# Kernel tuning notes

Measured on AMD Instinct MI355X. Metric: run time of the kernel, lower is better.

The kernel has to match this reference:

```python
import jax, jax.numpy as jnp
import numpy as np

SPATIAL_SCALE = 0.125  # stride-8 FPN level
POINTS = 5


def _sample_points(bb):
    # bb: [N,H,W,5] = (cx, cy, w, h, theta) in image coords
    cx, cy, w, h, t = [bb[..., i] for i in range(5)]
    if POINTS == 1:
        px = cx[..., None]
        py = cy[..., None]
    else:
        vx = w * jnp.cos(t) * 0.5
        vy = w * jnp.sin(t) * 0.5
        wx = -h * jnp.sin(t) * 0.5
        wy = h * jnp.cos(t) * 0.5
        px = jnp.stack([cx, cx + vx + wx, cx - vx + wx, cx - vx - wx, cx + vx - wx], axis=-1)
        py = jnp.stack([cy, cy + vy + wy, cy - vy + wy, cy - vy - wy, cy + vy - wy], axis=-1)
    return px * SPATIAL_SCALE, py * SPATIAL_SCALE  # [N,H,W,P] feature-map coords


def _bilinear_gather(feat, y, x):
    # feat: [N,C,H,W]; y,x: [N,H,W,P] -> [N,H,W,P,C], mmcv-style bilinear w/ border rules
    N, C, H, W = feat.shape
    valid = (y >= -1.0) & (y <= H) & (x >= -1.0) & (x <= W)
    y = jnp.maximum(y, 0.0)
    x = jnp.maximum(x, 0.0)
    y_low = jnp.minimum(jnp.floor(y).astype(jnp.int32), H - 1)
    x_low = jnp.minimum(jnp.floor(x).astype(jnp.int32), W - 1)
    # if low index hits last row/col, snap coordinate onto it (ly/lx = 0)
    y = jnp.where(y_low >= H - 1, y_low.astype(feat.dtype), y)
    x = jnp.where(x_low >= W - 1, x_low.astype(feat.dtype), x)
    y_high = jnp.minimum(y_low + 1, H - 1)
    x_high = jnp.minimum(x_low + 1, W - 1)
    ly = y - y_low.astype(feat.dtype)
    lx = x - x_low.astype(feat.dtype)
    hy = 1.0 - ly
    hx = 1.0 - lx
    nn = jnp.arange(N)[:, None, None, None]  # broadcasts against [N,H,W,P]

    def g(yy, xx):
        return feat[nn, :, yy, xx]  # [N,H,W,P,C]

    val = ((hy * hx)[..., None] * g(y_low, x_low)
           + (hy * lx)[..., None] * g(y_low, x_high)
           + (ly * hx)[..., None] * g(y_high, x_low)
           + (ly * lx)[..., None] * g(y_high, x_high))
    return jnp.where(valid[..., None], val, 0.0)


def feature_refine(features, best_rbboxes):
    px, py = _sample_points(best_rbboxes)
    sampled = _bilinear_gather(features, py, px)       # [N,H,W,P,C]
    acc = sampled.sum(axis=3)                           # [N,H,W,C]
    return features + jnp.transpose(acc, (0, 3, 1, 2))  # [N,C,H,W]


def setup_inputs() -> dict:
    key = jax.random.key(0)
    k1, k2, k3, k4, k5, k6 = jax.random.split(key, 6)
    N, C, H, W = 4, 256, 128, 128
    IMG = 1024.0
    features = jax.random.normal(k1, (N, C, H, W), dtype=jnp.float32)
    cx = jax.random.uniform(k2, (N, H, W), minval=0.0, maxval=IMG)
    cy = jax.random.uniform(k3, (N, H, W), minval=0.0, maxval=IMG)
    bw = jax.random.uniform(k4, (N, H, W), minval=8.0, maxval=128.0)
    bh = jax.random.uniform(k5, (N, H, W), minval=8.0, maxval=128.0)
    th = jax.random.uniform(k6, (N, H, W), minval=-np.pi / 2, maxval=np.pi / 2)
    best_rbboxes = jnp.stack([cx, cy, bw, bh, th], axis=-1)  # [N,H,W,5]
    return {"features": features, "best_rbboxes": best_rbboxes}


def reference(features, best_rbboxes):
    return feature_refine(features, best_rbboxes)
```

## Files before the change

### kernel.cpp

```cpp
#include <hip/hip_runtime.h>


#define N_ 4
#define C_ 256
#define H_ 128
#define W_ 128
#define HW_ (H_ * W_)
#define SCALE 0.125f

typedef unsigned int uint32;
typedef float f32x2 __attribute__((ext_vector_type(2)));

__device__ __forceinline__ uint32 f2bf(float f) {
    uint32 u = __float_as_uint(f);
    u = (u + 0x7FFF + ((u >> 16) & 1)) >> 16;
    return u;
}
__device__ __forceinline__ float blo(uint32 u) { return __uint_as_float(u << 16); }
__device__ __forceinline__ float bhi(uint32 u) { return __uint_as_float(u & 0xFFFF0000u); }

__global__ __launch_bounds__(1024, 8) void nchw2nhwc_geo(const float* __restrict__ in,
                                                         const float* __restrict__ bb,
                                                         uint32* __restrict__ outU,
                                                         uint32* __restrict__ geoG)
{
    __shared__ uint32 tile[64 * 260];
    const int t   = threadIdx.x;
    const int l   = t & 63;
    const int g   = t >> 6;
    const int hw0 = blockIdx.x * 256;
    const int ch  = blockIdx.y;
    const int n   = blockIdx.z;

    if (ch == 0 && t < 256) {
        const int px = n * HW_ + hw0 + t;
        const float* b = bb + (size_t)px * 5;
        const float cx = b[0], cy = b[1], bw = b[2], bh = b[3], th = b[4];
        const float st = sinf(th), ct = cosf(th);
        const float vx = bw * ct * 0.5f, vy = bw * st * 0.5f;
        const float wx = -bh * st * 0.5f, wy = bh * ct * 0.5f;
        const float pxs[5] = {cx, cx + vx + wx, cx - vx + wx, cx - vx - wx, cx + vx - wx};
        const float pys[5] = {cy, cy + vy + wy, cy - vy + wy, cy - vy - wy, cy + vy - wy};
        uint32* gw = geoG + (size_t)px * 40;
#pragma unroll
        for (int p = 0; p < 5; ++p) {
            float x = pxs[p] * SCALE;
            float y = pys[p] * SCALE;
            const bool valid = (y >= -1.0f) && (y <= (float)H_) &&
                               (x >= -1.0f) && (x <= (float)W_);
            y = fmaxf(y, 0.0f);
            x = fmaxf(x, 0.0f);
            int yl = min((int)y, H_ - 1);
            int xl = min((int)x, W_ - 1);
            if (yl >= H_ - 1) y = (float)yl;
            if (xl >= W_ - 1) x = (float)xl;
            const int yh = min(yl + 1, H_ - 1);
            const float ly = y - (float)yl, lx = x - (float)xl;
            const float hy = 1.0f - ly,     hx = 1.0f - lx;
            const int xa = min(xl, W_ - 2);
            float wA, wB;
            if (xl < W_ - 1) { wA = hx; wB = lx; }
            else             { wA = 0.0f; wB = 1.0f; }
            const float v = valid ? 1.0f : 0.0f;
            const int pix0 = yl * W_ + xa;
            const int pix1 = yh * W_ + xa;
            *(uint4*)&gw[p * 8]     = make_uint4((uint32)(pix0 * 512),
                                                 __float_as_uint(v * hy * wA),
                                                 (uint32)((pix0 + 1) * 512),
                                                 __float_as_uint(v * hy * wB));
            *(uint4*)&gw[p * 8 + 4] = make_uint4((uint32)(pix1 * 512),
                                                 __float_as_uint(v * ly * wA),
                                                 (uint32)((pix1 + 1) * 512),
                                                 __float_as_uint(v * ly * wB));
        }
    }

    const float* base = in + (size_t)n * C_ * HW_ + (size_t)(ch * 128) * HW_ + hw0 + 4 * l;
    float4 v0[4], v1[4];
#pragma unroll
    for (int r = 0; r < 4; ++r) {
        const int cp = g * 4 + r;
        v0[r] = *(const float4*)(base + (size_t)(2 * cp) * HW_);
        v1[r] = *(const float4*)(base + (size_t)(2 * cp + 1) * HW_);
    }
#pragma unroll
    for (int r = 0; r < 4; ++r) {
        const int cp = g * 4 + r;
        uint4 u;
        u.x = f2bf(v0[r].x) | (f2bf(v1[r].x) << 16);
        u.y = f2bf(v0[r].y) | (f2bf(v1[r].y) << 16);
        u.z = f2bf(v0[r].z) | (f2bf(v1[r].z) << 16);
        u.w = f2bf(v0[r].w) | (f2bf(v1[r].w) << 16);
        *(uint4*)&tile[cp * 260 + 4 * l] = u;
    }
    __syncthreads();
    uint32* dst = outU + ((size_t)n * HW_ + hw0) * 128 + ch * 64;
#pragma unroll
    for (int it = 0; it < 16; ++it) {
        const int f   = it * 1024 + t;
        const int row = f >> 6;
        const int q   = f & 63;
        dst[(size_t)row * 128 + q] = tile[q * 260 + row];
    }
}

__global__ __launch_bounds__(256, 8) void fr_refine(const uint32* __restrict__ nhwcU,
                                                    const uint32* __restrict__ geoG,
                                                    float* __restrict__ out)
{
    __shared__ float tile[32 * 128];
    const int t  = threadIdx.x;
    const int l  = t & 63;
    const int wv = __builtin_amdgcn_readfirstlane(t >> 6);
    const int bx = blockIdx.x;
    const int xcd = bx & 7;
    const int n   = xcd >> 1;
    const int ch  = xcd & 1;
    const int s   = bx >> 3;
    const int h   = s >> 2;
    const int w0  = (s & 3) * 32;

    const int k8   = (l >> 4) << 3;
    const int slot = (l & 15) << 4;
    const int hwb  = h * W_ + w0 + wv * 8;
    const char* gbase = (const char*)geoG + (size_t)(n * HW_ + hwb) * 160;
    const char* plane = (const char*)(nhwcU + (size_t)n * HW_ * 128) + (ch << 8);

#pragma unroll 1
    for (int p = 0; p < 8; ++p) {
        const char* gq = gbase + p * 160;

        uint2 ow[5];
#pragma unroll
        for (int q = 0; q < 5; ++q)
            ow[q] = *(const uint2*)(gq + q * 32 + k8);

        uint4 rid = make_uint4(0u, 0u, 0u, 0u);
        if (l < 16)
            rid = *(const uint4*)(plane + (size_t)(hwb + p) * 512 + slot);
        uint4 r[5];
#pragma unroll
        for (int q = 0; q < 5; ++q)
            r[q] = *(const uint4*)(plane + ow[q].x + slot);
        __builtin_amdgcn_sched_barrier(0);

        f32x2 acc0, acc1, acc2, acc3;
        acc0.x = blo(rid.x); acc0.y = bhi(rid.x);
        acc1.x = blo(rid.y); acc1.y = bhi(rid.y);
        acc2.x = blo(rid.z); acc2.y = bhi(rid.z);
        acc3.x = blo(rid.w); acc3.y = bhi(rid.w);
#pragma unroll
        for (int q = 0; q < 5; ++q) {
            const float w = __uint_as_float(ow[q].y);
            f32x2 w2; w2.x = w; w2.y = w;
            f32x2 u;
            u.x = blo(r[q].x); u.y = bhi(r[q].x); acc0 += u * w2;
            u.x = blo(r[q].y); u.y = bhi(r[q].y); acc1 += u * w2;
            u.x = blo(r[q].z); u.y = bhi(r[q].z); acc2 += u * w2;
            u.x = blo(r[q].w); u.y = bhi(r[q].w); acc3 += u * w2;
        }
        float a[8] = {acc0.x, acc0.y, acc1.x, acc1.y,
                      acc2.x, acc2.y, acc3.x, acc3.y};
#pragma unroll
        for (int k = 0; k < 8; ++k) {
            a[k] += __shfl_xor(a[k], 16, 64);
            a[k] += __shfl_xor(a[k], 32, 64);
        }
        if (l < 16) {
            const int px  = wv * 8 + p;
            const int swz = (px & 7) << 2;
            float* base = &tile[px * 128];
            *(float4*)&base[(l * 8) ^ swz]     = make_float4(a[0], a[1], a[2], a[3]);
            *(float4*)&base[(l * 8 + 4) ^ swz] = make_float4(a[4], a[5], a[6], a[7]);
        }
    }
    __syncthreads();
    const size_t obase = (size_t)n * C_ * HW_ + (size_t)(ch * 128) * HW_ + h * W_ + w0;
#pragma unroll
    for (int it = 0; it < 16; ++it) {
        const int flat = it * 256 + t;
        const int px = flat & 31;
        const int c  = flat >> 5;
        out[obase + (size_t)c * HW_ + px] = tile[px * 128 + (c ^ ((px & 7) << 2))];
    }
}

__global__ __launch_bounds__(256) void fr_kernel(
    const float* __restrict__ feat,
    const float* __restrict__ bb,
    float* __restrict__ out)
{
    const int lane = threadIdx.x & 63;
    const int wave = threadIdx.x >> 6;
    const int tile = blockIdx.x;
    const int wt   = tile & 1;
    const int h    = (tile >> 1) & (H_ - 1);
    const int n    = tile >> 8;
    const int w    = wt * 64 + lane;
    const int cb   = blockIdx.y;

    const float* b = bb + (size_t)((n * H_ + h) * W_ + w) * 5;
    const float cx = b[0], cy = b[1], bw = b[2], bh = b[3], th = b[4];
    const float st = sinf(th), ct = cosf(th);
    const float vx = bw * ct * 0.5f, vy = bw * st * 0.5f;
    const float wx = -bh * st * 0.5f, wy = bh * ct * 0.5f;
    const float pxs[5] = {cx, cx + vx + wx, cx - vx + wx, cx - vx - wx, cx + vx - wx};
    const float pys[5] = {cy, cy + vy + wy, cy - vy + wy, cy - vy - wy, cy + vy - wy};

    int   off0[5], off1[5];
    float wgt[20];
#pragma unroll
    for (int p = 0; p < 5; ++p) {
        float x = pxs[p] * SCALE;
        float y = pys[p] * SCALE;
        const bool valid = (y >= -1.0f) && (y <= (float)H_) &&
                           (x >= -1.0f) && (x <= (float)W_);
        y = fmaxf(y, 0.0f);
        x = fmaxf(x, 0.0f);
        int yl = min((int)y, H_ - 1);
        int xl = min((int)x, W_ - 1);
        if (yl >= H_ - 1) y = (float)yl;
        if (xl >= W_ - 1) x = (float)xl;
        const int yh = min(yl + 1, H_ - 1);
        const float ly = y - (float)yl, lx = x - (float)xl;
        const float hy = 1.0f - ly,     hx = 1.0f - lx;
        const int xa = min(xl, W_ - 2);
        float wA, wB;
        if (xl < W_ - 1) { wA = hx; wB = lx; }
        else             { wA = 0.0f; wB = 1.0f; }
        const float v = valid ? 1.0f : 0.0f;
        off0[p] = yl * W_ + xa;
        off1[p] = yh * W_ + xa;
        wgt[p * 4 + 0] = v * hy * wA;
        wgt[p * 4 + 1] = v * hy * wB;
        wgt[p * 4 + 2] = v * ly * wA;
        wgt[p * 4 + 3] = v * ly * wB;
    }

    const int hw = h * W_ + w;
    const size_t planeBase = ((size_t)n * C_ + cb * 64 + wave * 16) * HW_;
    const float* fp = feat + planeBase;
    float*       op = out  + planeBase;
    for (int it = 0; it < 16; ++it) {
        float acc = fp[hw];
#pragma unroll
        for (int p = 0; p < 5; ++p) {
            acc += wgt[p * 4 + 0] * fp[off0[p]]
                 + wgt[p * 4 + 1] * fp[off0[p] + 1]
                 + wgt[p * 4 + 2] * fp[off1[p]]
                 + wgt[p * 4 + 3] * fp[off1[p] + 1];
        }
        op[hw] = acc;
        fp += HW_;
        op += HW_;
    }
}

extern "C" void kernel_launch(void* const* d_in, const int* in_sizes, int n_in,
                              void* d_out, int out_size, void* d_ws, size_t ws_size,
                              hipStream_t stream) {
    const float* feat = (const float*)d_in[0];
    const float* bbox = (const float*)d_in[1];
    float* out = (float*)d_out;

    const size_t nhwcBytes = (size_t)N_ * HW_ * C_ * 2;
    const size_t geoBytes  = (size_t)N_ * HW_ * 160;
    if (ws_size >= nhwcBytes + geoBytes) {
        uint32* nhwcU = (uint32*)d_ws;
        uint32* geoG  = (uint32*)((char*)d_ws + nhwcBytes);
        nchw2nhwc_geo<<<dim3(HW_ / 256, 2, N_), dim3(1024), 0, stream>>>(feat, bbox, nhwcU, geoG);
        fr_refine<<<dim3(N_ * H_ * (W_ / 32) * 2), dim3(256), 0, stream>>>(nhwcU, geoG, out);
    } else {
        dim3 grid(N_ * H_ * (W_ / 64), C_ / 64, 1);
        fr_kernel<<<grid, dim3(256), 0, stream>>>(feat, bbox, out);
    }
}
```

Before: 167.4 us.

## Software-pipeline gather loads in refine kernel and vectorize NHWC transpose stores

The refine kernel's pixel loop is fully unrolled and software-pipelined. Geometry offsets are prefetched two iterations ahead and feature gathers one iteration ahead, so global-load latency overlaps the FMA and shuffle reduction of the current pixel. This raises register use, so launch bounds drop from 8 to 4 blocks per SM, trading occupancy for instruction-level overlap. Separately, the NCHW-to-NHWC transpose kernel now writes 16-byte uint4 stores in place of scalar stores, reducing store instruction count.

Result: no change. 166.5 us (-0.5%).

```diff
diff --git a/kernel.cpp b/kernel.cpp
--- a/kernel.cpp
+++ b/kernel.cpp
@@ -96,15 +96,19 @@
     __syncthreads();
     uint32* dst = outU + ((size_t)n * HW_ + hw0) * 128 + ch * 64;
 #pragma unroll
-    for (int it = 0; it < 16; ++it) {
-        const int f   = it * 1024 + t;
-        const int row = f >> 6;
-        const int q   = f & 63;
-        dst[(size_t)row * 128 + q] = tile[q * 260 + row];
-    }
-}
-
-__global__ __launch_bounds__(256, 8) void fr_refine(const uint32* __restrict__ nhwcU,
+    for (int it = 0; it < 4; ++it) {
+        const int px  = it * 64 + (t >> 4);
+        const int cp0 = (t & 15) * 4;
+        uint4 v;
+        v.x = tile[(cp0 + 0) * 260 + px];
+        v.y = tile[(cp0 + 1) * 260 + px];
+        v.z = tile[(cp0 + 2) * 260 + px];
+        v.w = tile[(cp0 + 3) * 260 + px];
+        *(uint4*)&dst[(size_t)px * 128 + cp0] = v;
+    }
+}
+
+__global__ __launch_bounds__(256, 4) void fr_refine(const uint32* __restrict__ nhwcU,
                                                     const uint32* __restrict__ geoG,
                                                     float* __restrict__ out)
 {
@@ -125,39 +129,52 @@
     const int hwb  = h * W_ + w0 + wv * 8;
     const char* gbase = (const char*)geoG + (size_t)(n * HW_ + hwb) * 160;
     const char* plane = (const char*)(nhwcU + (size_t)n * HW_ * 128) + (ch << 8);
-
-#pragma unroll 1
+    const bool idlane = (l < 16);
+
+    uint2 owA[5], owB[5], owC[5];
+    uint4 rA[5], rB[5];
+    uint4 ridA, ridB;
+
+#pragma unroll
+    for (int q = 0; q < 5; ++q) owA[q] = *(const uint2*)(gbase + q * 32 + k8);
+#pragma unroll
+    for (int q = 0; q < 5; ++q) owB[q] = *(const uint2*)(gbase + 160 + q * 32 + k8);
+    ridA = make_uint4(0u, 0u, 0u, 0u);
+    if (idlane) ridA = *(const uint4*)(plane + (size_t)hwb * 512 + slot);
+#pragma unroll
+    for (int q = 0; q < 5; ++q) rA[q] = *(const uint4*)(plane + owA[q].x + slot);
+    __builtin_amdgcn_sched_barrier(0);
+
+#pragma unroll
     for (int p = 0; p < 8; ++p) {
-        const char* gq = gbase + p * 160;
-
-        uint2 ow[5];
-#pragma unroll
-        for (int q = 0; q < 5; ++q)
-            ow[q] = *(const uint2*)(gq + q * 32 + k8);
-
-        uint4 rid = make_uint4(0u, 0u, 0u, 0u);
-        if (l < 16)
-            rid = *(const uint4*)(plane + (size_t)(hwb + p) * 512 + slot);
-        uint4 r[5];
-#pragma unroll
-        for (int q = 0; q < 5; ++q)
-            r[q] = *(const uint4*)(plane + ow[q].x + slot);
+        if (p + 2 < 8) {
+#pragma unroll
+            for (int q = 0; q < 5; ++q)
+                owC[q] = *(const uint2*)(gbase + (p + 2) * 160 + q * 32 + k8);
+        }
+        if (p + 1 < 8) {
+            ridB = make_uint4(0u, 0u, 0u, 0u);
+            if (idlane) ridB = *(const uint4*)(plane + (size_t)(hwb + p + 1) * 512 + slot);
+#pragma unroll
+            for (int q = 0; q < 5; ++q)
+                rB[q] = *(const uint4*)(plane + owB[q].x + slot);
+        }
         __builtin_amdgcn_sched_barrier(0);
 
         f32x2 acc0, acc1, acc2, acc3;
-        acc0.x = blo(rid.x); acc0.y = bhi(rid.x);
-        acc1.x = blo(rid.y); acc1.y = bhi(rid.y);
-        acc2.x = blo(rid.z); acc2.y = bhi(rid.z);
-        acc3.x = blo(rid.w); acc3.y = bhi(rid.w);
+        acc0.x = blo(ridA.x); acc0.y = bhi(ridA.x);
+        acc1.x = blo(ridA.y); acc1.y = bhi(ridA.y);
+        acc2.x = blo(ridA.z); acc2.y = bhi(ridA.z);
+        acc3.x = blo(ridA.w); acc3.y = bhi(ridA.w);
 #pragma unroll
         for (int q = 0; q < 5; ++q) {
-            const float w = __uint_as_float(ow[q].y);
+            const float w = __uint_as_float(owA[q].y);
             f32x2 w2; w2.x = w; w2.y = w;
             f32x2 u;
-            u.x = blo(r[q].x); u.y = bhi(r[q].x); acc0 += u * w2;
-            u.x = blo(r[q].y); u.y = bhi(r[q].y); acc1 += u * w2;
-            u.x = blo(r[q].z); u.y = bhi(r[q].z); acc2 += u * w2;
-            u.x = blo(r[q].w); u.y = bhi(r[q].w); acc3 += u * w2;
+            u.x = blo(rA[q].x); u.y = bhi(rA[q].x); acc0 += u * w2;
+            u.x = blo(rA[q].y); u.y = bhi(rA[q].y); acc1 += u * w2;
+            u.x = blo(rA[q].z); u.y = bhi(rA[q].z); acc2 += u * w2;
+            u.x = blo(rA[q].w); u.y = bhi(rA[q].w); acc3 += u * w2;
         }
         float a[8] = {acc0.x, acc0.y, acc1.x, acc1.y,
                       acc2.x, acc2.y, acc3.x, acc3.y};
@@ -166,13 +183,17 @@
             a[k] += __shfl_xor(a[k], 16, 64);
             a[k] += __shfl_xor(a[k], 32, 64);
         }
-        if (l < 16) {
+        if (idlane) {
             const int px  = wv * 8 + p;
             const int swz = (px & 7) << 2;
             float* base = &tile[px * 128];
             *(float4*)&base[(l * 8) ^ swz]     = make_float4(a[0], a[1], a[2], a[3]);
             *(float4*)&base[(l * 8 + 4) ^ swz] = make_float4(a[4], a[5], a[6], a[7]);
         }
+
+#pragma unroll
+        for (int q = 0; q < 5; ++q) { owA[q] = owB[q]; owB[q] = owC[q]; rA[q] = rB[q]; }
+        ridA = ridB;
     }
     __syncthreads();
     const size_t obase = (size_t)n * C_ * HW_ + (size_t)(ch * 128) * HW_ + h * W_ + w0;
```
